# Optimization experiments

Measured on AMD Instinct MI355X. Metric: run time of the kernel, lower is better.

The kernel has to match this reference:

```python
import jax, jax.numpy as jnp
import numpy as np

DIM = 1024
DEPTH = 6
HEADS = 16
FF = 4 * DIM
EPS = 1e-5


def _layernorm(x, g, b):
    mu = jnp.mean(x, axis=-1, keepdims=True)
    var = jnp.mean(jnp.square(x - mu), axis=-1, keepdims=True)
    return (x - mu) * jax.lax.rsqrt(var + EPS) * g + b


def setup_inputs() -> dict:
    key = jax.random.key(0)
    ks = jax.random.split(key, 16)
    s = 0.02
    inp = {
        "x": jax.random.normal(ks[0], (2, 1024, DIM), dtype=jnp.float32),
        "relative_position_bias": jax.random.normal(ks[1], (1, HEADS, 1024, 1024), dtype=jnp.float32),
        # stacked per-layer params [DEPTH, ...]
        "ln1_g": jnp.ones((DEPTH, DIM), jnp.float32),
        "ln1_b": jnp.zeros((DEPTH, DIM), jnp.float32),
        "w_qkv": jax.random.normal(ks[2], (DEPTH, DIM, 3 * DIM), dtype=jnp.float32) * s,
        "w_out": jax.random.normal(ks[3], (DEPTH, DIM, DIM), dtype=jnp.float32) * s,
        "b_out": jnp.zeros((DEPTH, DIM), jnp.float32),
        "ln2_g": jnp.ones((DEPTH, DIM), jnp.float32),
        "ln2_b": jnp.zeros((DEPTH, DIM), jnp.float32),
        "w1": jax.random.normal(ks[4], (DEPTH, DIM, FF), dtype=jnp.float32) * s,
        "b1": jnp.zeros((DEPTH, FF), jnp.float32),
        "w2": jax.random.normal(ks[5], (DEPTH, FF, DIM), dtype=jnp.float32) * s,
        "b2": jnp.zeros((DEPTH, DIM), jnp.float32),
    }
    return inp


def _forward(x, relative_position_bias, ln1_g, ln1_b, w_qkv, w_out, b_out,
             ln2_g, ln2_b, w1, b1, w2, b2):
    b, n, d = x.shape
    dh = d // HEADS
    scale = dh ** -0.5
    for l in range(DEPTH):
        # attention block (pre-norm)
        h = _layernorm(x, ln1_g[l], ln1_b[l])
        qkv = h @ w_qkv[l]                                    # [b, n, 3d]
        q, k, v = jnp.split(qkv, 3, axis=-1)
        q = q.reshape(b, n, HEADS, dh).transpose(0, 2, 1, 3)  # [b, h, n, dh]
        k = k.reshape(b, n, HEADS, dh).transpose(0, 2, 1, 3)
        v = v.reshape(b, n, HEADS, dh).transpose(0, 2, 1, 3)
        scores = jnp.einsum('bhid,bhjd->bhij', q, k) * scale + relative_position_bias
        attn = jax.nn.softmax(scores, axis=-1)
        o = jnp.einsum('bhij,bhjd->bhid', attn, v)
        o = o.transpose(0, 2, 1, 3).reshape(b, n, d)
        x = x + (o @ w_out[l] + b_out[l])
        # FFN block (pre-norm)
        h = _layernorm(x, ln2_g[l], ln2_b[l])
        h = jax.nn.gelu(h @ w1[l] + b1[l], approximate=False)
        x = x + (h @ w2[l] + b2[l])
    return x


def reference(x, relative_position_bias, ln1_g, ln1_b, w_qkv, w_out, b_out,
              ln2_g, ln2_b, w1, b1, w2, b2):
    return _forward(x, relative_position_bias, ln1_g, ln1_b, w_qkv, w_out, b_out,
                    ln2_g, ln2_b, w1, b1, w2, b2)
```

## Files before the change

### kernel.cpp

```cpp
#include <hip/hip_runtime.h>
#include <stdint.h>

#define DIM   1024
#define DEPTH 6
#define HEADS 16
#define FF    4096
#define SEQ   1024
#define BATCH 2
#define ROWS  (BATCH*SEQ)
#define DH    64

typedef __bf16 bf16x8 __attribute__((ext_vector_type(8)));
typedef float  f32x4  __attribute__((ext_vector_type(4)));

__device__ __forceinline__ unsigned short f2bf(float f) {
  unsigned int u = __builtin_bit_cast(unsigned int, f);
  u += 0x7fff + ((u >> 16) & 1);
  return (unsigned short)(u >> 16);
}
__device__ __forceinline__ float bf2f(unsigned short h) {
  unsigned int u = ((unsigned int)h) << 16;
  return __builtin_bit_cast(float, u);
}

__device__ __forceinline__ void async_load16(const void* g, void* l) {
  __builtin_amdgcn_global_load_lds(
      (const __attribute__((address_space(1))) unsigned int*)g,
      (__attribute__((address_space(3))) unsigned int*)l, 16, 0, 0);
}

template<int BM, int BN, int EPI, int NBUF, int MINW>
__global__ void __launch_bounds__(256, MINW)
gemm_kernel(const unsigned short* __restrict__ A, long lda,
            const unsigned short* __restrict__ B, long ldb,
            unsigned short* __restrict__ Cb, float* __restrict__ Cf, long ldc,
            const float* __restrict__ bias1, float scale, int K)
{
  constexpr int BK = 64;
  __shared__ unsigned short As[NBUF * BM * BK];
  __shared__ unsigned short Bs[NBUF * BN * BK];

  const int tid  = threadIdx.x;
  const int row0 = blockIdx.x * BM;
  const int col0 = blockIdx.y * BN;

  constexpr int WGN = 2;
  constexpr int WGM = 2;
  constexpr int WTM = BM / WGM;
  constexpr int WTN = BN / WGN;
  constexpr int ITM = WTM / 16;
  constexpr int ITN = WTN / 16;

  const int w = tid >> 6, l = tid & 63;
  const int quad = l >> 4, r16 = l & 15;
  const int wm = (w / WGN) * WTM;
  const int wn = (w % WGN) * WTN;
  const int sw = r16 & 7;

  f32x4 acc[ITM][ITN] = {};

  constexpr int APASS = (BM * 8) / 256;
  constexpr int BPASS = (BN * 8) / 256;

  const unsigned short* Ag = A + (long)row0 * lda;
  const unsigned short* Bg = B + (long)col0 * ldb;

  auto stage = [&](int buf, long k0) {
    unsigned short* Asb = &As[buf * (BM * BK)];
    unsigned short* Bsb = &Bs[buf * (BN * BK)];
#pragma unroll
    for (int p = 0; p < APASS; p++) {
      int flat = p * 256 + tid;
      int r = flat >> 3, cl = flat & 7;
      int cg = cl ^ (r & 7);
      async_load16(Ag + (long)r * lda + k0 + cg * 8, &Asb[flat * 8]);
    }
#pragma unroll
    for (int p = 0; p < BPASS; p++) {
      int flat = p * 256 + tid;
      int r = flat >> 3, cl = flat & 7;
      int cg = cl ^ (r & 7);
      async_load16(Bg + (long)r * ldb + k0 + cg * 8, &Bsb[flat * 8]);
    }
  };

  auto compute = [&](int buf) {
    const unsigned short* Asb = &As[buf * (BM * BK)];
    const unsigned short* Bsb = &Bs[buf * (BN * BK)];
#pragma unroll
    for (int ks = 0; ks < 2; ks++) {
      const int c = ks * 4 + quad;
      bf16x8 af[ITM], bfr[ITN];
#pragma unroll
      for (int i = 0; i < ITM; i++)
        af[i] = *(const bf16x8*)&Asb[(wm + i * 16 + r16) * BK + (c ^ sw) * 8];
#pragma unroll
      for (int j = 0; j < ITN; j++)
        bfr[j] = *(const bf16x8*)&Bsb[(wn + j * 16 + r16) * BK + (c ^ sw) * 8];
#pragma unroll
      for (int i = 0; i < ITM; i++)
#pragma unroll
        for (int j = 0; j < ITN; j++)
          acc[i][j] = __builtin_amdgcn_mfma_f32_16x16x32_bf16(af[i], bfr[j], acc[i][j], 0, 0, 0);
    }
  };

  if constexpr (NBUF == 1) {
    stage(0, 0);
    __syncthreads();
    compute(0);
  } else {
    stage(0, 0);
    __syncthreads();
    int cur = 0;
    for (long k0 = BK; k0 < K; k0 += BK) {
      stage(cur ^ 1, k0);
      compute(cur);
      __syncthreads();
      cur ^= 1;
    }
    compute(cur);
  }

#pragma unroll
  for (int i = 0; i < ITM; i++) {
#pragma unroll
    for (int j = 0; j < ITN; j++) {
      const int rr = row0 + wm + i * 16 + quad * 4;
      const int cc = col0 + wn + j * 16 + r16;
#pragma unroll
      for (int r = 0; r < 4; r++) {
        const long idx = (long)(rr + r) * ldc + cc;
        float v = acc[i][j][r];
        if constexpr (EPI == 0) {
          Cb[idx] = f2bf(v);
        } else if constexpr (EPI == 2) {
          Cf[idx] += v + bias1[cc];
        } else if constexpr (EPI == 3) {
          v += bias1[cc];
          float gl = 0.5f * v * (1.0f + erff(v * 0.70710678118654752f));
          Cb[idx] = f2bf(gl);
        }
      }
    }
  }
}

__global__ void __launch_bounds__(256, 2)
k_flashattn(const unsigned short* __restrict__ qkv,
            const unsigned short* __restrict__ vT,
            const unsigned short* __restrict__ rpbh,
            unsigned short* __restrict__ O)
{
  constexpr int QT = 64;
  constexpr int KT = 64;
  constexpr int NT = SEQ / KT;
  constexpr float SCL2 = 0.18033688f;
  constexpr float THR  = 11.5415603f;

  __shared__ __align__(16) unsigned short Qs[QT * DH];
  __shared__ __align__(16) unsigned short Ks[2][KT * DH];
  __shared__ __align__(16) unsigned short Vs[2][DH * KT];
  __shared__ __align__(16) unsigned short Ps[4][16 * KT];

  const int z = blockIdx.z;
  const int b_ = z >> 4, h_ = z & 15;
  const int q0 = blockIdx.x * QT;
  const int tid = threadIdx.x;
  const int w = tid >> 6, l = tid & 63;
  const int quad = l >> 4, r16 = l & 15;
  const int sw = r16 & 7;

  const unsigned short* Qg = qkv + (long)b_ * SEQ * (3 * DIM) + h_ * DH;
  const unsigned short* Kg = Qg + DIM;
  const unsigned short* Vg = vT + (long)z * DH * SEQ;
  const unsigned short* Rg = rpbh + (long)h_ * SEQ * SEQ + (long)q0 * SEQ;

  auto stageKV = [&](int buf, int kt) {
#pragma unroll
    for (int p = 0; p < 2; p++) {
      int flat = p * 256 + tid;
      int r = flat >> 3, cl = flat & 7, cg = cl ^ (r & 7);
      async_load16(Kg + (long)(kt * KT + r) * (3 * DIM) + cg * 8, &Ks[buf][flat * 8]);
    }
#pragma unroll
    for (int p = 0; p < 2; p++) {
      int flat = p * 256 + tid;
      int r = flat >> 3, cl = flat & 7, cg = cl ^ (r & 7);
      async_load16(Vg + (long)r * SEQ + kt * KT + cg * 8, &Vs[buf][flat * 8]);
    }
  };

#pragma unroll
  for (int p = 0; p < 2; p++) {
    int flat = p * 256 + tid;
    int r = flat >> 3, cl = flat & 7, cg = cl ^ (r & 7);
    async_load16(Qg + (long)(q0 + r) * (3 * DIM) + cg * 8, &Qs[flat * 8]);
  }
  stageKV(0, 0);
  __syncthreads();

  bf16x8 qA[2];
#pragma unroll
  for (int ks = 0; ks < 2; ks++)
    qA[ks] = *(const bf16x8*)&Qs[(w * 16 + r16) * DH + (((ks * 4 + quad)) ^ sw) * 8];

  f32x4 Oacc[4] = {};
  float m[4], lsum[4];
#pragma unroll
  for (int r = 0; r < 4; r++) { m[r] = -1e30f; lsum[r] = 0.0f; }

  int cur = 0;
  for (int kt = 0; kt < NT; kt++) {
    if (kt + 1 < NT) stageKV(cur ^ 1, kt + 1);

    float bias[4][4];
    const unsigned short* Rt = Rg + kt * KT;
#pragma unroll
    for (int j = 0; j < 4; j++)
#pragma unroll
      for (int r = 0; r < 4; r++)
        bias[j][r] = bf2f(Rt[(long)(w * 16 + quad * 4 + r) * SEQ + j * 16 + r16]);

    f32x4 s[4] = {};
#pragma unroll
    for (int ks = 0; ks < 2; ks++) {
      bf16x8 kB[4];
#pragma unroll
      for (int j = 0; j < 4; j++)
        kB[j] = *(const bf16x8*)&Ks[cur][(j * 16 + r16) * DH + ((ks * 4 + quad) ^ sw) * 8];
#pragma unroll
      for (int j = 0; j < 4; j++)
        s[j] = __builtin_amdgcn_mfma_f32_16x16x32_bf16(qA[ks], kB[j], s[j], 0, 0, 0);
    }

    float sc[4][4], p_[4][4], mt[4], ts[4];
#pragma unroll
    for (int j = 0; j < 4; j++)
#pragma unroll
      for (int r = 0; r < 4; r++)
        sc[j][r] = __builtin_fmaf(s[j][r], SCL2, bias[j][r]);
#pragma unroll
    for (int r = 0; r < 4; r++) {
      mt[r] = fmaxf(fmaxf(sc[0][r], sc[1][r]), fmaxf(sc[2][r], sc[3][r]));
#pragma unroll
      for (int msk = 1; msk < 16; msk <<= 1)
        mt[r] = fmaxf(mt[r], __shfl_xor(mt[r], msk));
      if (mt[r] > m[r] + THR) {
        const float rs = __builtin_amdgcn_exp2f(m[r] - mt[r]);
        m[r] = mt[r];
#pragma unroll
        for (int j = 0; j < 4; j++) Oacc[j][r] *= rs;
        lsum[r] *= rs;
      }
#pragma unroll
      for (int j = 0; j < 4; j++)
        p_[j][r] = __builtin_amdgcn_exp2f(sc[j][r] - m[r]);
      ts[r] = p_[0][r] + p_[1][r] + p_[2][r] + p_[3][r];
#pragma unroll
      for (int msk = 1; msk < 16; msk <<= 1)
        ts[r] += __shfl_xor(ts[r], msk);
      lsum[r] += ts[r];
    }

    unsigned short* Pw = &Ps[w][0];
#pragma unroll
    for (int j = 0; j < 4; j++)
#pragma unroll
      for (int r = 0; r < 4; r++) {
        int row = quad * 4 + r;
        int col = j * 16 + r16;
        int chunk = col >> 3;
        Pw[row * KT + ((chunk ^ (row & 7)) * 8 + (col & 7))] = f2bf(p_[j][r]);
      }

#pragma unroll
    for (int ks = 0; ks < 2; ks++) {
      bf16x8 pA = *(const bf16x8*)&Pw[r16 * KT + ((ks * 4 + quad) ^ sw) * 8];
      bf16x8 vB[4];
#pragma unroll
      for (int j = 0; j < 4; j++)
        vB[j] = *(const bf16x8*)&Vs[cur][(j * 16 + r16) * KT + ((ks * 4 + quad) ^ sw) * 8];
#pragma unroll
      for (int j = 0; j < 4; j++)
        Oacc[j] = __builtin_amdgcn_mfma_f32_16x16x32_bf16(pA, vB[j], Oacc[j], 0, 0, 0);
    }

    __syncthreads();
    cur ^= 1;
  }

#pragma unroll
  for (int r = 0; r < 4; r++) {
    const float inv = 1.0f / lsum[r];
    const long rowg = (long)b_ * SEQ + q0 + w * 16 + quad * 4 + r;
#pragma unroll
    for (int j = 0; j < 4; j++)
      O[rowg * DIM + h_ * DH + j * 16 + r16] = f2bf(Oacc[j][r] * inv);
  }
}

__global__ void k_layernorm(const float* __restrict__ x, const float* __restrict__ g,
                            const float* __restrict__ b, unsigned short* __restrict__ out)
{
  const int row = blockIdx.x;
  const int t = threadIdx.x;
  float4 v = ((const float4*)(x + (long)row * DIM))[t];
  float s = v.x + v.y + v.z + v.w;
  float q = v.x * v.x + v.y * v.y + v.z * v.z + v.w * v.w;
#pragma unroll
  for (int off = 32; off > 0; off >>= 1) {
    s += __shfl_down(s, off);
    q += __shfl_down(q, off);
  }
  __shared__ float shs[4], shq[4];
  if ((t & 63) == 0) { shs[t >> 6] = s; shq[t >> 6] = q; }
  __syncthreads();
  s = shs[0] + shs[1] + shs[2] + shs[3];
  q = shq[0] + shq[1] + shq[2] + shq[3];
  const float mu  = s * (1.0f / DIM);
  const float var = q * (1.0f / DIM) - mu * mu;
  const float rs  = rsqrtf(var + 1e-5f);
  float4 gg = ((const float4*)g)[t];
  float4 bb = ((const float4*)b)[t];
  ushort4 o;
  o.x = f2bf((v.x - mu) * rs * gg.x + bb.x);
  o.y = f2bf((v.y - mu) * rs * gg.y + bb.y);
  o.z = f2bf((v.z - mu) * rs * gg.z + bb.z);
  o.w = f2bf((v.w - mu) * rs * gg.w + bb.w);
  ((ushort4*)out)[(long)row * (DIM / 4) + t] = o;
}

__global__ void k_cvtrpb(const float* __restrict__ src, unsigned short* __restrict__ dst)
{
  const long i = ((long)blockIdx.x * 256 + threadIdx.x) * 4;
  float4 v = *(const float4*)(src + i);
  ushort4 o;
  o.x = f2bf(v.x * 1.44269504f);
  o.y = f2bf(v.y * 1.44269504f);
  o.z = f2bf(v.z * 1.44269504f);
  o.w = f2bf(v.w * 1.44269504f);
  *(ushort4*)(dst + i) = o;
}

__global__ void k_wtrans_all(const float* __restrict__ wqkv, const float* __restrict__ wout,
                             const float* __restrict__ w1,   const float* __restrict__ w2,
                             unsigned short* __restrict__ wTqkv, unsigned short* __restrict__ wTout,
                             unsigned short* __restrict__ wT1,   unsigned short* __restrict__ wT2)
{
  __shared__ unsigned short tile[64][65];
  int t = blockIdx.x;
  const float* w; unsigned short* wT; int K, N;
  if (t < 768)        {            w = wqkv; wT = wTqkv; K = DIM; N = 3 * DIM; }
  else if (t < 1024)  { t -= 768;  w = wout; wT = wTout; K = DIM; N = DIM; }
  else if (t < 2048)  { t -= 1024; w = w1;   wT = wT1;   K = DIM; N = FF; }
  else                { t -= 2048; w = w2;   wT = wT2;   K = FF;  N = DIM; }
  const int nt = N / 64;
  const int n0 = (t % nt) * 64, k0 = (t / nt) * 64;
  const int tx = threadIdx.x, ty = threadIdx.y;
#pragma unroll
  for (int i = 0; i < 16; i++)
    tile[ty + 4 * i][tx] = f2bf(w[(long)(k0 + ty + 4 * i) * N + n0 + tx]);
  __syncthreads();
#pragma unroll
  for (int i = 0; i < 16; i++)
    wT[(long)(n0 + ty + 4 * i) * K + k0 + tx] = tile[tx][ty + 4 * i];
}

__global__ void k_vtrans(const unsigned short* __restrict__ qkv, unsigned short* __restrict__ vT)
{
  __shared__ unsigned short tile[64][65];
  const int z = blockIdx.z;
  const int b_ = z >> 4, h_ = z & 15;
  const int n0 = blockIdx.x * 64;
  const int tx = threadIdx.x, ty = threadIdx.y;
  const unsigned short* src = qkv + (long)b_ * SEQ * (3 * DIM) + 2 * DIM + h_ * DH;
#pragma unroll
  for (int i = 0; i < 16; i++)
    tile[ty + 4 * i][tx] = src[(long)(n0 + ty + 4 * i) * (3 * DIM) + tx];
  __syncthreads();
  unsigned short* dst = vT + (long)z * DH * SEQ;
#pragma unroll
  for (int i = 0; i < 16; i++)
    dst[(long)(ty + 4 * i) * SEQ + n0 + tx] = tile[tx][ty + 4 * i];
}

extern "C" void kernel_launch(void* const* d_in, const int* in_sizes, int n_in,
                              void* d_out, int out_size, void* d_ws, size_t ws_size,
                              hipStream_t stream)
{
  const float* x0   = (const float*)d_in[0];
  const float* rpb  = (const float*)d_in[1];
  const float* ln1g = (const float*)d_in[2];
  const float* ln1b = (const float*)d_in[3];
  const float* wqkv = (const float*)d_in[4];
  const float* wout = (const float*)d_in[5];
  const float* bout = (const float*)d_in[6];
  const float* ln2g = (const float*)d_in[7];
  const float* ln2b = (const float*)d_in[8];
  const float* w1   = (const float*)d_in[9];
  const float* b1   = (const float*)d_in[10];
  const float* w2   = (const float*)d_in[11];
  const float* b2   = (const float*)d_in[12];
  float* x = (float*)d_out;

  char* p = (char*)d_ws;
  auto alloc = [&](size_t n) { char* r = p; p += (n + 255) & ~(size_t)255; return r; };
  unsigned short* wTqkv = (unsigned short*)alloc((size_t)3 * DIM * DIM * 2);
  unsigned short* wTout = (unsigned short*)alloc((size_t)DIM * DIM * 2);
  unsigned short* wT1   = (unsigned short*)alloc((size_t)FF * DIM * 2);
  unsigned short* wT2   = (unsigned short*)alloc((size_t)DIM * FF * 2);
  unsigned short* hbuf  = (unsigned short*)alloc((size_t)ROWS * DIM * 2);
  unsigned short* qkvb  = (unsigned short*)alloc((size_t)ROWS * 3 * DIM * 2);
  unsigned short* vTb   = (unsigned short*)alloc((size_t)BATCH * HEADS * DH * SEQ * 2);
  unsigned short* obuf  = (unsigned short*)alloc((size_t)ROWS * DIM * 2);
  unsigned short* ffnb  = (unsigned short*)alloc((size_t)ROWS * FF * 2);
  unsigned short* rpbh  = (unsigned short*)alloc((size_t)HEADS * SEQ * SEQ * 2);

  hipMemcpyAsync(x, x0, (size_t)ROWS * DIM * 4, hipMemcpyDeviceToDevice, stream);

  k_cvtrpb<<<dim3(16384), 256, 0, stream>>>(rpb, rpbh);

  const dim3 tb(64, 4);
  for (int l = 0; l < DEPTH; l++) {
    const float* Wqkv = wqkv + (size_t)l * DIM * 3 * DIM;
    const float* Wout = wout + (size_t)l * DIM * DIM;
    const float* W1   = w1   + (size_t)l * DIM * FF;
    const float* W2   = w2   + (size_t)l * FF * DIM;

    k_wtrans_all<<<dim3(3072), tb, 0, stream>>>(Wqkv, Wout, W1, W2,
                                                wTqkv, wTout, wT1, wT2);

    k_layernorm<<<ROWS, 256, 0, stream>>>(x, ln1g + l * DIM, ln1b + l * DIM, hbuf);

    gemm_kernel<64, 128, 0, 2, 4><<<dim3(ROWS / 64, 3 * DIM / 128), 256, 0, stream>>>(
        hbuf, DIM, wTqkv, DIM, qkvb, nullptr, 3 * DIM, nullptr, 1.0f, DIM);

    k_vtrans<<<dim3(SEQ / 64, 1, BATCH * HEADS), tb, 0, stream>>>(qkvb, vTb);

    k_flashattn<<<dim3(SEQ / 64, 1, BATCH * HEADS), 256, 0, stream>>>(
        qkvb, vTb, rpbh, obuf);

    gemm_kernel<64, 64, 2, 2, 4><<<dim3(ROWS / 64, DIM / 64), 256, 0, stream>>>(
        obuf, DIM, wTout, DIM, nullptr, x, DIM, bout + l * DIM, 1.0f, DIM);

    k_layernorm<<<ROWS, 256, 0, stream>>>(x, ln2g + l * DIM, ln2b + l * DIM, hbuf);

    gemm_kernel<128, 128, 3, 2, 2><<<dim3(ROWS / 128, FF / 128), 256, 0, stream>>>(
        hbuf, DIM, wT1, DIM, ffnb, nullptr, FF, b1 + l * FF, 1.0f, DIM);

    gemm_kernel<64, 64, 2, 2, 4><<<dim3(ROWS / 64, DIM / 64), 256, 0, stream>>>(
        ffnb, FF, wT2, FF, nullptr, x, DIM, b2 + l * DIM, 1.0f, FF);
  }
}
```

Measured before the change: 1.346 ms.

## Add split-K to residual GEMMs, drop double buffering, shrink tiles to 64x64

The output-projection and FFN-down GEMMs now split K into two halves across blockIdx.z. Each half writes fp32 partials to a scratch buffer, and a new reduce kernel adds both partials plus the bias into the residual. The GEMM loses its LDS double-buffered pipeline and becomes a simple load-sync-compute loop. QKV and FFN-up tiles shrink to 64x64 to raise block count and occupancy. The trade is more blocks and parallelism for extra partial-buffer traffic, an extra launch, and no overlap of global loads with MFMA.

```diff
diff --git a/kernel.cpp b/kernel.cpp
--- a/kernel.cpp
+++ b/kernel.cpp
@@ -29,16 +29,20 @@
       (__attribute__((address_space(3))) unsigned int*)l, 16, 0, 0);
 }
 
-template<int BM, int BN, int EPI, int NBUF, int MINW>
+template<int BM, int BN, int EPI, int SPLITK, int MINW>
 __global__ void __launch_bounds__(256, MINW)
 gemm_kernel(const unsigned short* __restrict__ A, long lda,
             const unsigned short* __restrict__ B, long ldb,
             unsigned short* __restrict__ Cb, float* __restrict__ Cf, long ldc,
-            const float* __restrict__ bias1, float scale, int K)
+            const float* __restrict__ bias1, int K, long pstride)
 {
   constexpr int BK = 64;
-  __shared__ unsigned short As[NBUF * BM * BK];
-  __shared__ unsigned short Bs[NBUF * BN * BK];
+  const int z = blockIdx.z;
+  const int Kloc = K / SPLITK;
+  const long kbase = (long)z * Kloc;
+
+  __shared__ unsigned short As[BM * BK];
+  __shared__ unsigned short Bs[BN * BK];
 
   const int tid  = threadIdx.x;
   const int row0 = blockIdx.x * BM;
@@ -65,61 +69,39 @@
   const unsigned short* Ag = A + (long)row0 * lda;
   const unsigned short* Bg = B + (long)col0 * ldb;
 
-  auto stage = [&](int buf, long k0) {
-    unsigned short* Asb = &As[buf * (BM * BK)];
-    unsigned short* Bsb = &Bs[buf * (BN * BK)];
+  for (long k0 = kbase; k0 < kbase + Kloc; k0 += BK) {
 #pragma unroll
     for (int p = 0; p < APASS; p++) {
       int flat = p * 256 + tid;
       int r = flat >> 3, cl = flat & 7;
       int cg = cl ^ (r & 7);
-      async_load16(Ag + (long)r * lda + k0 + cg * 8, &Asb[flat * 8]);
+      async_load16(Ag + (long)r * lda + k0 + cg * 8, &As[flat * 8]);
     }
 #pragma unroll
     for (int p = 0; p < BPASS; p++) {
       int flat = p * 256 + tid;
       int r = flat >> 3, cl = flat & 7;
       int cg = cl ^ (r & 7);
-      async_load16(Bg + (long)r * ldb + k0 + cg * 8, &Bsb[flat * 8]);
-    }
-  };
-
-  auto compute = [&](int buf) {
-    const unsigned short* Asb = &As[buf * (BM * BK)];
-    const unsigned short* Bsb = &Bs[buf * (BN * BK)];
+      async_load16(Bg + (long)r * ldb + k0 + cg * 8, &Bs[flat * 8]);
+    }
+    __syncthreads();
 #pragma unroll
     for (int ks = 0; ks < 2; ks++) {
       const int c = ks * 4 + quad;
       bf16x8 af[ITM], bfr[ITN];
 #pragma unroll
       for (int i = 0; i < ITM; i++)
-        af[i] = *(const bf16x8*)&Asb[(wm + i * 16 + r16) * BK + (c ^ sw) * 8];
+        af[i] = *(const bf16x8*)&As[(wm + i * 16 + r16) * BK + (c ^ sw) * 8];
 #pragma unroll
       for (int j = 0; j < ITN; j++)
-        bfr[j] = *(const bf16x8*)&Bsb[(wn + j * 16 + r16) * BK + (c ^ sw) * 8];
+        bfr[j] = *(const bf16x8*)&Bs[(wn + j * 16 + r16) * BK + (c ^ sw) * 8];
 #pragma unroll
       for (int i = 0; i < ITM; i++)
 #pragma unroll
         for (int j = 0; j < ITN; j++)
           acc[i][j] = __builtin_amdgcn_mfma_f32_16x16x32_bf16(af[i], bfr[j], acc[i][j], 0, 0, 0);
     }
-  };
-
-  if constexpr (NBUF == 1) {
-    stage(0, 0);
     __syncthreads();
-    compute(0);
-  } else {
-    stage(0, 0);
-    __syncthreads();
-    int cur = 0;
-    for (long k0 = BK; k0 < K; k0 += BK) {
-      stage(cur ^ 1, k0);
-      compute(cur);
-      __syncthreads();
-      cur ^= 1;
-    }
-    compute(cur);
   }
 
 #pragma unroll
@@ -134,16 +116,31 @@
         float v = acc[i][j][r];
         if constexpr (EPI == 0) {
           Cb[idx] = f2bf(v);
-        } else if constexpr (EPI == 2) {
-          Cf[idx] += v + bias1[cc];
         } else if constexpr (EPI == 3) {
           v += bias1[cc];
           float gl = 0.5f * v * (1.0f + erff(v * 0.70710678118654752f));
           Cb[idx] = f2bf(gl);
+        } else if constexpr (EPI == 4) {
+          Cf[(long)z * pstride + idx] = v;
         }
       }
     }
   }
+}
+
+__global__ void k_reduce2(float* __restrict__ x, const float* __restrict__ pbuf,
+                          const float* __restrict__ bias)
+{
+  const long i = (long)blockIdx.x * 256 + threadIdx.x;
+  float4 a  = ((float4*)x)[i];
+  float4 p0 = ((const float4*)pbuf)[i];
+  float4 p1 = ((const float4*)(pbuf + (long)ROWS * DIM))[i];
+  float4 bb = ((const float4*)bias)[i & (DIM / 4 - 1)];
+  a.x += p0.x + p1.x + bb.x;
+  a.y += p0.y + p1.y + bb.y;
+  a.z += p0.z + p1.z + bb.z;
+  a.w += p0.w + p1.w + bb.w;
+  ((float4*)x)[i] = a;
 }
 
 __global__ void __launch_bounds__(256, 2)
@@ -416,12 +413,14 @@
   unsigned short* obuf  = (unsigned short*)alloc((size_t)ROWS * DIM * 2);
   unsigned short* ffnb  = (unsigned short*)alloc((size_t)ROWS * FF * 2);
   unsigned short* rpbh  = (unsigned short*)alloc((size_t)HEADS * SEQ * SEQ * 2);
+  float*          pbuf  = (float*)alloc((size_t)2 * ROWS * DIM * 4);
 
   hipMemcpyAsync(x, x0, (size_t)ROWS * DIM * 4, hipMemcpyDeviceToDevice, stream);
 
   k_cvtrpb<<<dim3(16384), 256, 0, stream>>>(rpb, rpbh);
 
   const dim3 tb(64, 4);
+  const long PS = (long)ROWS * DIM;
   for (int l = 0; l < DEPTH; l++) {
     const float* Wqkv = wqkv + (size_t)l * DIM * 3 * DIM;
     const float* Wout = wout + (size_t)l * DIM * DIM;
@@ -433,23 +432,25 @@
 
     k_layernorm<<<ROWS, 256, 0, stream>>>(x, ln1g + l * DIM, ln1b + l * DIM, hbuf);
 
-    gemm_kernel<64, 128, 0, 2, 4><<<dim3(ROWS / 64, 3 * DIM / 128), 256, 0, stream>>>(
-        hbuf, DIM, wTqkv, DIM, qkvb, nullptr, 3 * DIM, nullptr, 1.0f, DIM);
+    gemm_kernel<64, 64, 0, 1, 4><<<dim3(ROWS / 64, 3 * DIM / 64), 256, 0, stream>>>(
+        hbuf, DIM, wTqkv, DIM, qkvb, nullptr, 3 * DIM, nullptr, DIM, 0);
 
     k_vtrans<<<dim3(SEQ / 64, 1, BATCH * HEADS), tb, 0, stream>>>(qkvb, vTb);
 
     k_flashattn<<<dim3(SEQ / 64, 1, BATCH * HEADS), 256, 0, stream>>>(
         qkvb, vTb, rpbh, obuf);
 
-    gemm_kernel<64, 64, 2, 2, 4><<<dim3(ROWS / 64, DIM / 64), 256, 0, stream>>>(
-        obuf, DIM, wTout, DIM, nullptr, x, DIM, bout + l * DIM, 1.0f, DIM);
+    gemm_kernel<64, 64, 4, 2, 4><<<dim3(ROWS / 64, DIM / 64, 2), 256, 0, stream>>>(
+        obuf, DIM, wTout, DIM, nullptr, pbuf, DIM, nullptr, DIM, PS);
+    k_reduce2<<<dim3(ROWS * DIM / 1024), 256, 0, stream>>>(x, pbuf, bout + l * DIM);
 
     k_layernorm<<<ROWS, 256, 0, stream>>>(x, ln2g + l * DIM, ln2b + l * DIM, hbuf);
 
-    gemm_kernel<128, 128, 3, 2, 2><<<dim3(ROWS / 128, FF / 128), 256, 0, stream>>>(
-        hbuf, DIM, wT1, DIM, ffnb, nullptr, FF, b1 + l * FF, 1.0f, DIM);
-
-    gemm_kernel<64, 64, 2, 2, 4><<<dim3(ROWS / 64, DIM / 64), 256, 0, stream>>>(
-        ffnb, FF, wT2, FF, nullptr, x, DIM, b2 + l * DIM, 1.0f, FF);
-  }
-}
+    gemm_kernel<64, 64, 3, 1, 4><<<dim3(ROWS / 64, FF / 64), 256, 0, stream>>>(
+        hbuf, DIM, wT1, DIM, ffnb, nullptr, FF, b1 + l * FF, DIM, 0);
+
+    gemm_kernel<64, 64, 4, 2, 4><<<dim3(ROWS / 64, DIM / 64, 2), 256, 0, stream>>>(
+        ffnb, FF, wT2, FF, nullptr, pbuf, DIM, nullptr, FF, PS);
+    k_reduce2<<<dim3(ROWS * DIM / 1024), 256, 0, stream>>>(x, pbuf, b2 + l * DIM);
+  }
+}
```

New measurement: 1.278 ms. -5.1%, faster.
